# Kernel optimization log

Measured on AMD Instinct MI355X. Metric: run time of the kernel, lower is better.

Reference implementation:

```python
import jax, jax.numpy as jnp
import numpy as np

B, S, H, HS, BLK = 4, 4096, 16, 1024, 64
D = HS // H


def setup_inputs() -> dict:
    key = jax.random.key(0)
    ks = jax.random.split(key, 7)
    s = np.float32(1.0 / np.sqrt(HS))
    return {
        "hidden_states": jax.random.normal(ks[0], (B, S, HS), jnp.float32),
        "Wq": jax.random.normal(ks[1], (HS, HS), jnp.float32) * s,
        "bq": jax.random.normal(ks[2], (HS,), jnp.float32) * s,
        "Wk": jax.random.normal(ks[3], (HS, HS), jnp.float32) * s,
        "bk": jax.random.normal(ks[4], (HS,), jnp.float32) * s,
        "Wv": jax.random.normal(ks[5], (HS, HS), jnp.float32) * s,
        "bv": jax.random.normal(ks[6], (HS,), jnp.float32) * s,
    }


def reference(hidden_states, Wq, bq, Wk, bk, Wv, bv):
    b, m, _ = hidden_states.shape
    h, d, wm = H, D, BLK
    wn = wm
    nb = m // wm  # number of blocks
    scale = np.float32(1.0 / np.sqrt(d))

    def heads(x):  # [b, m, hs] -> [b, h, m, d]
        return x.reshape(b, m, h, d).transpose(0, 2, 1, 3)

    q = heads(hidden_states @ Wq.T + bq)
    k = heads(hidden_states @ Wk.T + bk)
    v = heads(hidden_states @ Wv.T + bv)

    qb = q.reshape(b, h, nb, wm, d)
    kb = k.reshape(b, h, nb, wn, d)
    vb = v.reshape(b, h, nb, wn, d)

    def attend(qx, kx, vx):  # qx [b,h,Q,d], kx/vx [b,h,K,d]
        scores = jnp.einsum('bhqd,bhkd->bhqk', qx, kx) * scale
        return jnp.einsum('bhqk,bhkd->bhqd', jax.nn.softmax(scores, axis=-1), vx)

    # first block: full attention over all keys
    first_ctx = attend(qb[:, :, 0], k, v)[:, :, None]

    # second block: keys = blocks [0, 1, 2, -1]
    k2 = jnp.concatenate([kb[:, :, 0], kb[:, :, 1], kb[:, :, 2], kb[:, :, -1]], axis=2)
    v2 = jnp.concatenate([vb[:, :, 0], vb[:, :, 1], vb[:, :, 2], vb[:, :, -1]], axis=2)
    second_ctx = attend(qb[:, :, 1], k2, v2)[:, :, None]

    # middle blocks 2..nb-3: sliding window of 3 key blocks + global first/last
    exp_k = jnp.concatenate([kb[:, :, 1:-3], kb[:, :, 2:-2], kb[:, :, 3:-1]], axis=3)  # [b,h,l,3wn,d]
    exp_v = jnp.concatenate([vb[:, :, 1:-3], vb[:, :, 2:-2], vb[:, :, 3:-1]], axis=3)
    mq = qb[:, :, 2:-2]  # [b,h,l,wm,d]
    inner = jnp.einsum('bhlqd,bhlkd->bhlqk', mq, exp_k) * scale
    first_band = jnp.einsum('bhlqd,bhkd->bhlqk', mq, kb[:, :, 0]) * scale
    last_band = jnp.einsum('bhlqd,bhkd->bhlqk', mq, kb[:, :, -1]) * scale
    band = jnp.concatenate([first_band, inner, last_band], axis=-1)  # [b,h,l,wm,5wn]
    aw = jax.nn.softmax(band, axis=-1)
    mid_ctx = jnp.einsum('bhlqk,bhlkd->bhlqd', aw[..., wn:4 * wn], exp_v)
    mid_ctx = mid_ctx + jnp.einsum('bhlqk,bhkd->bhlqd', aw[..., :wn], vb[:, :, 0])
    mid_ctx = mid_ctx + jnp.einsum('bhlqk,bhkd->bhlqd', aw[..., -wn:], vb[:, :, -1])

    # second-to-last block: keys = blocks [0, -3, -2, -1]
    k3 = jnp.concatenate([kb[:, :, 0], kb[:, :, -3], kb[:, :, -2], kb[:, :, -1]], axis=2)
    v3 = jnp.concatenate([vb[:, :, 0], vb[:, :, -3], vb[:, :, -2], vb[:, :, -1]], axis=2)
    second_last_ctx = attend(qb[:, :, -2], k3, v3)[:, :, None]

    # last block: full attention over all keys
    last_ctx = attend(qb[:, :, -1], k, v)[:, :, None]

    ctx = jnp.concatenate([first_ctx, second_ctx, mid_ctx, second_last_ctx, last_ctx], axis=2)
    return ctx.reshape(b, h, m, d).transpose(0, 2, 1, 3).reshape(b, m, h * d)
```

## Files before the change

### kernel.cpp

```cpp
#include <hip/hip_runtime.h>

typedef unsigned short u16;
using f32x4  = __attribute__((ext_vector_type(4))) float;
using bf16x8 = __attribute__((ext_vector_type(8))) short;

#define SEQ 4096
#define HS  1024
#define NHEAD 16
#define DH  64

__device__ __forceinline__ u16 f2bf(float f) {
  unsigned u = __float_as_uint(f);
  unsigned r = (u + 0x7fffu + ((u >> 16) & 1u)) >> 16;
  return (u16)r;
}

__device__ __forceinline__ void gl_lds16(const void* g, void* l) {
  __builtin_amdgcn_global_load_lds(
      (const __attribute__((address_space(1))) unsigned int*)g,
      (__attribute__((address_space(3))) unsigned int*)l, 16, 0, 0);
}

__global__ void cvt_kernel(const float* __restrict__ src, u16* __restrict__ dst, int n) {
  int idx = blockIdx.x * blockDim.x + threadIdx.x;
  int stride = gridDim.x * blockDim.x;
  for (int i = idx * 4; i < n; i += stride * 4) {
    float4 v = *reinterpret_cast<const float4*>(src + i);
    u16 o0 = f2bf(v.x), o1 = f2bf(v.y), o2 = f2bf(v.z), o3 = f2bf(v.w);
    unsigned lo = (unsigned)o0 | ((unsigned)o1 << 16);
    unsigned hi = (unsigned)o2 | ((unsigned)o3 << 16);
    uint2 pk; pk.x = lo; pk.y = hi;
    *reinterpret_cast<uint2*>(dst + i) = pk;
  }
}

__global__ void cvt_w_kernel(const float* __restrict__ w0, const float* __restrict__ w1,
                             const float* __restrict__ w2,
                             u16* __restrict__ d0, u16* __restrict__ d1, u16* __restrict__ d2,
                             int n) {
  const float* s; u16* d;
  if (blockIdx.y == 0) { s = w0; d = d0; }
  else if (blockIdx.y == 1) { s = w1; d = d1; }
  else { s = w2; d = d2; }
  int idx = blockIdx.x * blockDim.x + threadIdx.x;
  int stride = gridDim.x * blockDim.x;
  for (int i = idx * 4; i < n; i += stride * 4) {
    float4 v = *reinterpret_cast<const float4*>(s + i);
    u16 o0 = f2bf(v.x), o1 = f2bf(v.y), o2 = f2bf(v.z), o3 = f2bf(v.w);
    unsigned lo = (unsigned)o0 | ((unsigned)o1 << 16);
    unsigned hi = (unsigned)o2 | ((unsigned)o3 << 16);
    uint2 pk; pk.x = lo; pk.y = hi;
    *reinterpret_cast<uint2*>(d + i) = pk;
  }
}

__global__ void gemm_qkv(const u16* __restrict__ X,
                         const u16* __restrict__ Wq, const u16* __restrict__ Wk,
                         const u16* __restrict__ Wv,
                         const float* __restrict__ bq, const float* __restrict__ bk,
                         const float* __restrict__ bv,
                         u16* __restrict__ Q, u16* __restrict__ K, u16* __restrict__ V) {
  const u16* W; const float* bias; u16* O;
  if (blockIdx.z == 0)      { W = Wq; bias = bq; O = Q; }
  else if (blockIdx.z == 1) { W = Wk; bias = bk; O = K; }
  else                      { W = Wv; bias = bv; O = V; }

  __shared__ u16 As[128 * 64];
  __shared__ u16 Bs[128 * 64];

  const int tid = threadIdx.x;
  const int lane = tid & 63;
  const int w = tid >> 6;
  const int wr = w >> 1, wc = w & 1;
  const int m0 = blockIdx.x * 128;
  const int n0 = blockIdx.y * 128;

  f32x4 acc[4][4] = {};

  const int srow = lane >> 3;
  const int scol = (lane & 7) * 8;

  for (int k0 = 0; k0 < HS; k0 += 64) {
#pragma unroll
    for (int t = 0; t < 4; ++t) {
      int sub = w * 4 + t;
      int r = sub * 8 + srow;
      gl_lds16(X + (size_t)(m0 + r) * HS + k0 + scol, As + sub * 512);
      gl_lds16(W + (size_t)(n0 + r) * HS + k0 + scol, Bs + sub * 512);
    }
    __syncthreads();
#pragma unroll
    for (int ks = 0; ks < 2; ++ks) {
      bf16x8 a[4], b[4];
#pragma unroll
      for (int mf = 0; mf < 4; ++mf)
        a[mf] = *reinterpret_cast<const bf16x8*>(
            As + (wr * 64 + mf * 16 + (lane & 15)) * 64 + ks * 32 + (lane >> 4) * 8);
#pragma unroll
      for (int nf = 0; nf < 4; ++nf)
        b[nf] = *reinterpret_cast<const bf16x8*>(
            Bs + (wc * 64 + nf * 16 + (lane & 15)) * 64 + ks * 32 + (lane >> 4) * 8);
#pragma unroll
      for (int mf = 0; mf < 4; ++mf)
#pragma unroll
        for (int nf = 0; nf < 4; ++nf)
          acc[mf][nf] = __builtin_amdgcn_mfma_f32_16x16x32_bf16(a[mf], b[nf], acc[mf][nf], 0, 0, 0);
    }
    __syncthreads();
  }

#pragma unroll
  for (int nf = 0; nf < 4; ++nf) {
    int cc = n0 + wc * 64 + nf * 16 + (lane & 15);
    float bval = bias[cc];
#pragma unroll
    for (int mf = 0; mf < 4; ++mf) {
#pragma unroll
      for (int j = 0; j < 4; ++j) {
        int r = m0 + wr * 64 + mf * 16 + (lane >> 4) * 4 + j;
        O[(size_t)r * HS + cc] = f2bf(acc[mf][nf][j] + bval);
      }
    }
  }
}

__global__ void bigbird_attn2(const u16* __restrict__ Q, const u16* __restrict__ K,
                              const u16* __restrict__ V, float* __restrict__ OUT,
                              float* __restrict__ Opart, float* __restrict__ MLpart) {
  __shared__ u16 Qs[64 * 64];
  __shared__ u16 Ks[2][64 * 64];
  __shared__ u16 Vt[64 * 72];
  __shared__ u16 Ps[64 * 72];

  const int tid = threadIdx.x;
  const int lane = tid & 63;
  const int w = tid >> 6;
  const int g = lane >> 4;
  const int c = lane & 15;

  int bid = blockIdx.x;
  int qb, b, h, nkb, seg4 = 0, p = 0;
  bool heavy;
  if (bid < 3968) {
    heavy = false;
    b = bid & 3; int t = bid >> 2; h = t & 15; qb = (t >> 4) + 1;
    nkb = (qb == 1 || qb == 62) ? 4 : 5;
  } else {
    heavy = true;
    int t = bid - 3968;
    b = t & 3; t >>= 2; h = t & 15; t >>= 4;
    int seg = t & 15; int q2 = t >> 4;
    qb = q2 ? 63 : 0; seg4 = seg * 4; nkb = 4;
    p = ((q2 * 16 + h) * 4 + b) * 16 + seg;
  }

  const size_t base_bh = (size_t)b * SEQ * HS + (size_t)h * DH;

  auto kb_of = [&](int it) -> int {
    if (heavy) return seg4 + it;
    if (qb == 1)  return (it == 3) ? 63 : it;
    if (qb == 62) return (it == 0) ? 0 : 60 + it;
    return (it == 0) ? 0 : ((it == 4) ? 63 : qb - 2 + it);
  };

  {
    const u16* qg = Q + base_bh + (size_t)qb * 64 * HS;
#pragma unroll
    for (int t2 = 0; t2 < 2; ++t2) {
      int sub = w * 2 + t2;
      int r = sub * 8 + (lane >> 3);
      int c16 = (lane & 7) ^ (r & 7);
      gl_lds16(qg + (size_t)r * HS + c16 * 8, Qs + sub * 512);
    }
  }
  int kb0 = kb_of(0);
  {
    const u16* kg = K + base_bh + (size_t)kb0 * 64 * HS;
#pragma unroll
    for (int t2 = 0; t2 < 2; ++t2) {
      int sub = w * 2 + t2;
      int r = sub * 8 + (lane >> 3);
      int c16 = (lane & 7) ^ (r & 7);
      gl_lds16(kg + (size_t)r * HS + c16 * 8, Ks[0] + sub * 512);
    }
  }
  bf16x8 vr0, vr1;
  {
    const u16* vg = V + base_bh + (size_t)kb0 * 64 * HS;
    int krow = tid >> 2, dseg = (tid & 3) * 16;
    vr0 = *reinterpret_cast<const bf16x8*>(vg + (size_t)krow * HS + dseg);
    vr1 = *reinterpret_cast<const bf16x8*>(vg + (size_t)krow * HS + dseg + 8);
  }
  __syncthreads();

  bf16x8 qf[2];
#pragma unroll
  for (int ks = 0; ks < 2; ++ks) {
    int r = w * 16 + c;
    int c16 = (ks * 4 + g) ^ (r & 7);
    qf[ks] = *reinterpret_cast<const bf16x8*>(Qs + r * 64 + c16 * 8);
  }

  float m_run = -1e30f, l_run = 0.f;
  f32x4 o_acc[4] = {};
  const float scale = 0.125f;

  for (int it = 0; it < nkb; ++it) {
    const int cur = it & 1;
    {
      int krow = tid >> 2, dseg = (tid & 3) * 16;
#pragma unroll
      for (int j2 = 0; j2 < 8; ++j2) {
        Vt[(dseg + j2) * 72 + krow]     = (u16)vr0[j2];
        Vt[(dseg + 8 + j2) * 72 + krow] = (u16)vr1[j2];
      }
    }
    if (it + 1 < nkb) {
      int kbn = kb_of(it + 1);
      const u16* kg = K + base_bh + (size_t)kbn * 64 * HS;
#pragma unroll
      for (int t2 = 0; t2 < 2; ++t2) {
        int sub = w * 2 + t2;
        int r = sub * 8 + (lane >> 3);
        int c16 = (lane & 7) ^ (r & 7);
        gl_lds16(kg + (size_t)r * HS + c16 * 8, Ks[cur ^ 1] + sub * 512);
      }
      const u16* vg = V + base_bh + (size_t)kbn * 64 * HS;
      int krow = tid >> 2, dseg = (tid & 3) * 16;
      vr0 = *reinterpret_cast<const bf16x8*>(vg + (size_t)krow * HS + dseg);
      vr1 = *reinterpret_cast<const bf16x8*>(vg + (size_t)krow * HS + dseg + 8);
    }

    f32x4 accs[4] = {};
#pragma unroll
    for (int ks = 0; ks < 2; ++ks) {
#pragma unroll
      for (int mf = 0; mf < 4; ++mf) {
        int r = mf * 16 + c;
        int c16 = (ks * 4 + g) ^ (r & 7);
        bf16x8 kf = *reinterpret_cast<const bf16x8*>(Ks[cur] + r * 64 + c16 * 8);
        accs[mf] = __builtin_amdgcn_mfma_f32_16x16x32_bf16(kf, qf[ks], accs[mf], 0, 0, 0);
      }
    }

    float sv[16];
    float smax = -1e30f;
#pragma unroll
    for (int mf = 0; mf < 4; ++mf)
#pragma unroll
      for (int j = 0; j < 4; ++j) {
        float s = accs[mf][j] * scale;
        sv[mf * 4 + j] = s;
        smax = fmaxf(smax, s);
      }
    smax = fmaxf(smax, __shfl_xor(smax, 16));
    smax = fmaxf(smax, __shfl_xor(smax, 32));
    float m_new = fmaxf(m_run, smax);
    float corr = __expf(m_run - m_new);
    float psum = 0.f;
    u16 pb[16];
#pragma unroll
    for (int i = 0; i < 16; ++i) {
      float pv = __expf(sv[i] - m_new);
      psum += pv;
      pb[i] = f2bf(pv);
    }
    psum += __shfl_xor(psum, 16);
    psum += __shfl_xor(psum, 32);
    l_run = l_run * corr + psum;
    m_run = m_new;

#pragma unroll
    for (int j = 0; j < 4; ++j) {
      float cj = __shfl(corr, g * 4 + j);
#pragma unroll
      for (int df = 0; df < 4; ++df) o_acc[df][j] *= cj;
    }

    {
      int r = w * 16 + c;
#pragma unroll
      for (int mf = 0; mf < 4; ++mf) {
        unsigned lo = (unsigned)pb[mf * 4 + 0] | ((unsigned)pb[mf * 4 + 1] << 16);
        unsigned hi = (unsigned)pb[mf * 4 + 2] | ((unsigned)pb[mf * 4 + 3] << 16);
        uint2 pk; pk.x = lo; pk.y = hi;
        *reinterpret_cast<uint2*>(Ps + r * 72 + mf * 16 + g * 4) = pk;
      }
    }

    __syncthreads();

#pragma unroll
    for (int ks = 0; ks < 2; ++ks) {
      bf16x8 pf = *reinterpret_cast<const bf16x8*>(Ps + (w * 16 + c) * 72 + ks * 32 + g * 8);
#pragma unroll
      for (int df = 0; df < 4; ++df) {
        bf16x8 vf = *reinterpret_cast<const bf16x8*>(Vt + (df * 16 + c) * 72 + ks * 32 + g * 8);
        o_acc[df] = __builtin_amdgcn_mfma_f32_16x16x32_bf16(pf, vf, o_acc[df], 0, 0, 0);
      }
    }

    __syncthreads();
  }

  if (!heavy) {
#pragma unroll
    for (int j = 0; j < 4; ++j) {
      float lr = __shfl(l_run, g * 4 + j);
      float inv = 1.f / lr;
      int r = qb * 64 + w * 16 + g * 4 + j;
      size_t rowbase = ((size_t)b * SEQ + r) * HS + (size_t)h * DH;
#pragma unroll
      for (int df = 0; df < 4; ++df)
        OUT[rowbase + df * 16 + c] = o_acc[df][j] * inv;
    }
  } else {
#pragma unroll
    for (int j = 0; j < 4; ++j) {
      int row = w * 16 + g * 4 + j;
#pragma unroll
      for (int df = 0; df < 4; ++df)
        Opart[(size_t)p * 4096 + row * 64 + df * 16 + c] = o_acc[df][j];
    }
    if (g == 0) {
      int row = w * 16 + c;
      MLpart[(size_t)p * 128 + row * 2]     = m_run;
      MLpart[(size_t)p * 128 + row * 2 + 1] = l_run;
    }
  }
}

__global__ void bigbird_combine(const float* __restrict__ Opart, const float* __restrict__ MLpart,
                                float* __restrict__ OUT) {
  int bid = blockIdx.x;
  int b = bid & 3; int t = bid >> 2; int h = t & 15; int q2 = t >> 4;
  int qb = q2 ? 63 : 0;
  int w = threadIdx.x >> 6, lane = threadIdx.x & 63;
  int pbase = ((q2 * 16 + h) * 4 + b) * 16;
#pragma unroll 1
  for (int rr = 0; rr < 16; ++rr) {
    int row = w * 16 + rr;
    float ms[16], ls[16];
    float M = -1e30f;
#pragma unroll
    for (int s = 0; s < 16; ++s) {
      ms[s] = MLpart[(size_t)(pbase + s) * 128 + row * 2];
      ls[s] = MLpart[(size_t)(pbase + s) * 128 + row * 2 + 1];
      M = fmaxf(M, ms[s]);
    }
    float L = 0.f, acc = 0.f;
#pragma unroll
    for (int s = 0; s < 16; ++s) {
      float e = __expf(ms[s] - M);
      L += ls[s] * e;
      acc += e * Opart[(size_t)(pbase + s) * 4096 + row * 64 + lane];
    }
    int r = qb * 64 + row;
    OUT[((size_t)b * SEQ + r) * HS + (size_t)h * DH + lane] = acc / L;
  }
}

extern "C" void kernel_launch(void* const* d_in, const int* in_sizes, int n_in,
                              void* d_out, int out_size, void* d_ws, size_t ws_size,
                              hipStream_t stream) {
  const float* X  = (const float*)d_in[0];
  const float* Wq = (const float*)d_in[1];
  const float* bq = (const float*)d_in[2];
  const float* Wk = (const float*)d_in[3];
  const float* bk = (const float*)d_in[4];
  const float* Wv = (const float*)d_in[5];
  const float* bv = (const float*)d_in[6];
  float* out = (float*)d_out;

  u16* Xb  = (u16*)d_ws;
  u16* Wqb = Xb + 16777216;
  u16* Wkb = Wqb + 1048576;
  u16* Wvb = Wkb + 1048576;
  u16* Qb  = Wvb + 1048576;
  u16* Kb  = Qb + 16777216;
  u16* Vb  = Kb + 16777216;

  float* Opart  = (float*)Xb;
  float* MLpart = (float*)Wqb;

  cvt_kernel<<<2048, 256, 0, stream>>>(X, Xb, 16777216);
  cvt_w_kernel<<<dim3(256, 3), 256, 0, stream>>>(Wq, Wk, Wv, Wqb, Wkb, Wvb, 1048576);
  gemm_qkv<<<dim3(128, 8, 3), 256, 0, stream>>>(Xb, Wqb, Wkb, Wvb, bq, bk, bv, Qb, Kb, Vb);
  bigbird_attn2<<<6016, 256, 0, stream>>>(Qb, Kb, Vb, out, Opart, MLpart);
  bigbird_combine<<<128, 256, 0, stream>>>(Opart, MLpart, out);
}
```

Baseline: 254.8 us.

## Rewrite QKV GEMM with 256x256 tiles, 8 waves, double-buffered pipelined LDS

Replaces the 128x128, 4-wave QKV projection GEMM with a 256x256 tile kernel using 8 waves and a 128KB double-buffered LDS split into K-halves. The next K-tile is prefetched while the current one is computed, and fine-grained vmcnt/lgkmcnt waits and barriers interleave loads with MFMA work. It also adds an XOR-swizzled LDS layout to avoid bank conflicts, a block-index swizzle for L2 locality, and s_setprio around the MFMA bursts. The goal is to hide global-load latency and raise MFMA utilisation, at the cost of lower occupancy from the large LDS footprint and fragile manual synchronisation.

Result: no change. 259.9 us (+2.0%).

```diff
diff --git a/kernel.cpp b/kernel.cpp
--- a/kernel.cpp
+++ b/kernel.cpp
@@ -20,6 +20,9 @@
       (const __attribute__((address_space(1))) unsigned int*)g,
       (__attribute__((address_space(3))) unsigned int*)l, 16, 0, 0);
 }
+
+#define LGKM0 asm volatile("s_waitcnt lgkmcnt(0)" ::: "memory")
+#define BARR  __builtin_amdgcn_s_barrier()
 
 __global__ void cvt_kernel(const float* __restrict__ src, u16* __restrict__ dst, int n) {
   int idx = blockIdx.x * blockDim.x + threadIdx.x;
@@ -54,73 +57,109 @@
   }
 }
 
-__global__ void gemm_qkv(const u16* __restrict__ X,
-                         const u16* __restrict__ Wq, const u16* __restrict__ Wk,
-                         const u16* __restrict__ Wv,
-                         const float* __restrict__ bq, const float* __restrict__ bk,
-                         const float* __restrict__ bv,
-                         u16* __restrict__ Q, u16* __restrict__ K, u16* __restrict__ V) {
+__global__ __launch_bounds__(512) void gemm_qkv8(
+    const u16* __restrict__ X,
+    const u16* __restrict__ Wq, const u16* __restrict__ Wk, const u16* __restrict__ Wv,
+    const float* __restrict__ bq, const float* __restrict__ bk, const float* __restrict__ bv,
+    u16* __restrict__ Q, u16* __restrict__ K, u16* __restrict__ V) {
   const u16* W; const float* bias; u16* O;
   if (blockIdx.z == 0)      { W = Wq; bias = bq; O = Q; }
   else if (blockIdx.z == 1) { W = Wk; bias = bk; O = K; }
   else                      { W = Wv; bias = bv; O = V; }
 
-  __shared__ u16 As[128 * 64];
-  __shared__ u16 Bs[128 * 64];
+  __shared__ u16 lds[65536];
 
   const int tid = threadIdx.x;
-  const int lane = tid & 63;
+  const int l = tid & 63;
   const int w = tid >> 6;
-  const int wr = w >> 1, wc = w & 1;
-  const int m0 = blockIdx.x * 128;
-  const int n0 = blockIdx.y * 128;
-
-  f32x4 acc[4][4] = {};
-
-  const int srow = lane >> 3;
-  const int scol = (lane & 7) * 8;
-
-  for (int k0 = 0; k0 < HS; k0 += 64) {
-#pragma unroll
-    for (int t = 0; t < 4; ++t) {
-      int sub = w * 4 + t;
-      int r = sub * 8 + srow;
-      gl_lds16(X + (size_t)(m0 + r) * HS + k0 + scol, As + sub * 512);
-      gl_lds16(W + (size_t)(n0 + r) * HS + k0 + scol, Bs + sub * 512);
-    }
-    __syncthreads();
-#pragma unroll
-    for (int ks = 0; ks < 2; ++ks) {
-      bf16x8 a[4], b[4];
+  const int wr = w >> 2;
+  const int wc = w & 3;
+  const int c = l & 15;
+  const int g = l >> 4;
+
+  int flat = blockIdx.x;
+  int swz = (flat & 7) * 32 + (flat >> 3);
+  const int n0 = (swz >> 6) * 256;
+  const int m0 = (swz & 63) * 256;
+
+  f32x4 acc[2][4][4] = {};
+
+  auto stage = [&](const u16* G, int gbase, int ktile, int kh, int which) {
+    u16* region = lds + ((ktile & 1) * 32768 + which * 16384 + kh * 8192);
+#pragma unroll
+    for (int i = 0; i < 2; ++i) {
+      int chunk = w * 2 + i;
+      int srow = chunk * 8 + (l >> 3);
+      int slot = (l & 7) ^ (l >> 3);
+      int grow = srow + ((slot >> 2) << 7);
+      int ke = ktile * 64 + kh * 32 + (slot & 3) * 8;
+      gl_lds16(G + (size_t)(gbase + grow) * HS + ke, region + chunk * 512);
+    }
+  };
+
+  auto readA = [&](int cur, int CH, int KH, bf16x8* aq) {
+    const char* base = (const char*)lds + cur * 65536 + KH * 16384;
+    int colb = (wr * 64 + g * 16) ^ ((c & 7) << 4);
+#pragma unroll
+    for (int mf = 0; mf < 4; ++mf)
+      aq[mf] = *reinterpret_cast<const bf16x8*>(base + (CH * 64 + mf * 16 + c) * 128 + colb);
+  };
+  auto readB = [&](int cur, int KH, bf16x8* bq) {
+    const char* base = (const char*)lds + cur * 65536 + 32768 + KH * 16384;
+    int colb = ((wc >> 1) * 64 + g * 16) ^ ((c & 7) << 4);
+#pragma unroll
+    for (int nf = 0; nf < 4; ++nf)
+      bq[nf] = *reinterpret_cast<const bf16x8*>(base + ((wc & 1) * 64 + nf * 16 + c) * 128 + colb);
+  };
+  auto mma16 = [&](bf16x8* aq, bf16x8* bq, f32x4 (*accr)[4]) {
+    __builtin_amdgcn_s_setprio(1);
+#pragma unroll
+    for (int mf = 0; mf < 4; ++mf)
+#pragma unroll
+      for (int nf = 0; nf < 4; ++nf)
+        accr[mf][nf] = __builtin_amdgcn_mfma_f32_16x16x32_bf16(aq[mf], bq[nf], accr[mf][nf], 0, 0, 0);
+    __builtin_amdgcn_s_setprio(0);
+  };
+
+  stage(X, m0, 0, 0, 0); stage(W, n0, 0, 0, 1);
+  stage(X, m0, 0, 1, 0); stage(W, n0, 0, 1, 1);
+  stage(X, m0, 1, 0, 0); stage(W, n0, 1, 0, 1);
+  asm volatile("s_waitcnt vmcnt(4)" ::: "memory");
+  BARR;
+
+  for (int j = 0; j < 16; ++j) {
+    const int cur = j & 1;
+    bf16x8 aq[4], bq[4];
+    readA(cur, 0, 0, aq); readB(cur, 0, bq);
+    if (j + 1 < 16) stage(X, m0, j + 1, 1, 0);
+    BARR; LGKM0; mma16(aq, bq, acc[0]); BARR;
+    readA(cur, 1, 0, aq);
+    if (j + 1 < 16) stage(W, n0, j + 1, 1, 1);
+    BARR; LGKM0; mma16(aq, bq, acc[1]); BARR;
+    readA(cur, 0, 1, aq); readB(cur, 1, bq);
+    if (j + 2 < 16) stage(X, m0, j + 2, 0, 0);
+    BARR; LGKM0; mma16(aq, bq, acc[0]); BARR;
+    readA(cur, 1, 1, aq);
+    if (j + 2 < 16) stage(W, n0, j + 2, 0, 1);
+    BARR; LGKM0; mma16(aq, bq, acc[1]);
+    if (j < 14)       asm volatile("s_waitcnt vmcnt(4)" ::: "memory");
+    else if (j == 14) asm volatile("s_waitcnt vmcnt(0)" ::: "memory");
+    BARR;
+  }
+
+#pragma unroll
+  for (int nf = 0; nf < 4; ++nf) {
+    int cc = n0 + wc * 64 + nf * 16 + c;
+    float bval = bias[cc];
+#pragma unroll
+    for (int ch = 0; ch < 2; ++ch)
 #pragma unroll
       for (int mf = 0; mf < 4; ++mf)
-        a[mf] = *reinterpret_cast<const bf16x8*>(
-            As + (wr * 64 + mf * 16 + (lane & 15)) * 64 + ks * 32 + (lane >> 4) * 8);
-#pragma unroll
-      for (int nf = 0; nf < 4; ++nf)
-        b[nf] = *reinterpret_cast<const bf16x8*>(
-            Bs + (wc * 64 + nf * 16 + (lane & 15)) * 64 + ks * 32 + (lane >> 4) * 8);
-#pragma unroll
-      for (int mf = 0; mf < 4; ++mf)
-#pragma unroll
-        for (int nf = 0; nf < 4; ++nf)
-          acc[mf][nf] = __builtin_amdgcn_mfma_f32_16x16x32_bf16(a[mf], b[nf], acc[mf][nf], 0, 0, 0);
-    }
-    __syncthreads();
-  }
-
-#pragma unroll
-  for (int nf = 0; nf < 4; ++nf) {
-    int cc = n0 + wc * 64 + nf * 16 + (lane & 15);
-    float bval = bias[cc];
-#pragma unroll
-    for (int mf = 0; mf < 4; ++mf) {
-#pragma unroll
-      for (int j = 0; j < 4; ++j) {
-        int r = m0 + wr * 64 + mf * 16 + (lane >> 4) * 4 + j;
-        O[(size_t)r * HS + cc] = f2bf(acc[mf][nf][j] + bval);
-      }
-    }
+#pragma unroll
+        for (int jj = 0; jj < 4; ++jj) {
+          int r = m0 + wr * 128 + ch * 64 + mf * 16 + g * 4 + jj;
+          O[(size_t)r * HS + cc] = f2bf(acc[ch][mf][nf][jj] + bval);
+        }
   }
 }
 
@@ -385,7 +424,7 @@
 
   cvt_kernel<<<2048, 256, 0, stream>>>(X, Xb, 16777216);
   cvt_w_kernel<<<dim3(256, 3), 256, 0, stream>>>(Wq, Wk, Wv, Wqb, Wkb, Wvb, 1048576);
-  gemm_qkv<<<dim3(128, 8, 3), 256, 0, stream>>>(Xb, Wqb, Wkb, Wvb, bq, bk, bv, Qb, Kb, Vb);
+  gemm_qkv8<<<dim3(256, 1, 3), 512, 0, stream>>>(Xb, Wqb, Wkb, Wvb, bq, bk, bv, Qb, Kb, Vb);
   bigbird_attn2<<<6016, 256, 0, stream>>>(Qb, Kb, Vb, out, Opart, MLpart);
   bigbird_combine<<<128, 256, 0, stream>>>(Opart, MLpart, out);
 }
```
